# Kernel optimization log

Measured on AMD Instinct MI355X. Metric: run time of the kernel, lower is better.

Reference implementation:

```python
import jax, jax.numpy as jnp
import numpy as np

B, T, D = 4, 2048, 1024
H = 16
HD = D // H  # 64

def setup_inputs() -> dict:
    key = jax.random.key(0)
    ks = jax.random.split(key, 7)
    s = 1.0 / np.sqrt(D)
    x = jax.random.normal(ks[0], (B, T, D), dtype=jnp.float32)
    # Per-head query projections stacked: Wq[h] maps D -> HD
    Wq = jax.random.uniform(ks[1], (H, D, HD), minval=-s, maxval=s, dtype=jnp.float32)
    bq = jax.random.uniform(ks[2], (H, HD), minval=-s, maxval=s, dtype=jnp.float32)
    Wk = jax.random.uniform(ks[3], (D, HD), minval=-s, maxval=s, dtype=jnp.float32)
    bk = jax.random.uniform(ks[4], (HD,), minval=-s, maxval=s, dtype=jnp.float32)
    Wv = jax.random.uniform(ks[5], (D, HD), minval=-s, maxval=s, dtype=jnp.float32)
    bv = jax.random.uniform(ks[6], (HD,), minval=-s, maxval=s, dtype=jnp.float32)
    return {"x": x, "Wq": Wq, "bq": bq, "Wk": Wk, "bk": bk, "Wv": Wv, "bv": bv}

def reference(x, Wq, bq, Wk, bk, Wv, bv):
    # shared single K/V head: [B, T, HD]
    k = jnp.einsum('btd,de->bte', x, Wk) + bk
    v = jnp.einsum('btd,de->bte', x, Wv) + bv
    # per-head queries batched: [B, H, T, HD]
    q = jnp.einsum('btd,hde->bhte', x, Wq) + bq[:, None, :]
    scale = 1.0 / jnp.sqrt(jnp.asarray(HD, dtype=x.dtype))
    scores = jnp.einsum('bhqe,bke->bhqk', q, k) * scale  # [B, H, T, T]
    attn = jax.nn.softmax(scores, axis=-1)
    out = jnp.einsum('bhqk,bke->bhqe', attn, v)  # [B, H, T, HD]
    # concat heads along last dim (head order matches torch cat order)
    return jnp.transpose(out, (0, 2, 1, 3)).reshape(B, T, H * HD)
```

## Files before the change

kernel.cpp:

```cpp
#include <hip/hip_runtime.h>

#define B 4
#define T 2048
#define D 1024
#define H 16
#define HD 64
#define NKT 32

typedef __attribute__((ext_vector_type(8))) short bf16x8;
typedef __attribute__((ext_vector_type(4))) float f32x4;
typedef __attribute__((ext_vector_type(16))) float f32x16;

#define MFMA16(a, b, c) __builtin_amdgcn_mfma_f32_16x16x32_bf16(a, b, c, 0, 0, 0)
#define MFMA32(a, b, c) __builtin_amdgcn_mfma_f32_32x32x16_bf16(a, b, c, 0, 0, 0)

static __device__ __forceinline__ unsigned short f2bf(float f) {
    union { float f; unsigned u; } v; v.f = f;
    unsigned r = v.u + 0x7FFFu + ((v.u >> 16) & 1u);
    return (unsigned short)(r >> 16);
}

static __device__ __forceinline__ bf16x8 cvt8(const float* p) {
    float4 a = *(const float4*)p;
    float4 b = *(const float4*)(p + 4);
    bf16x8 r;
    r[0] = (short)f2bf(a.x); r[1] = (short)f2bf(a.y);
    r[2] = (short)f2bf(a.z); r[3] = (short)f2bf(a.w);
    r[4] = (short)f2bf(b.x); r[5] = (short)f2bf(b.y);
    r[6] = (short)f2bf(b.z); r[7] = (short)f2bf(b.w);
    return r;
}

static __device__ __forceinline__ unsigned cvtpk(float lo, float hi) {
    unsigned r;
    asm("v_cvt_pk_bf16_f32 %0, %1, %2" : "=v"(r) : "v"(lo), "v"(hi));
    return r;
}

static __device__ __forceinline__ f32x16 zero16() {
    f32x16 z;
#pragma unroll
    for (int i = 0; i < 16; ++i) z[i] = 0.f;
    return z;
}

static __device__ __forceinline__ float xhalf_sum(float x) {
    unsigned u = __float_as_uint(x);
    auto r = __builtin_amdgcn_permlane32_swap(u, u, false, false);
    return __uint_as_float(r[0]) + __uint_as_float(r[1]);
}

typedef __attribute__((address_space(1))) const unsigned char gl_u8;
typedef __attribute__((address_space(3))) unsigned char lds_u8;

static __device__ __forceinline__ void stage16(const void* g, void* l) {
    __builtin_amdgcn_global_load_lds((gl_u8*)(unsigned long long)g,
                                     (lds_u8*)(unsigned int)(unsigned long long)l,
                                     16, 0, 0);
}

__global__ __launch_bounds__(256) void pack_w(const float* __restrict__ Wq,
                                              const float* __restrict__ Wk,
                                              const float* __restrict__ Wv,
                                              unsigned short* __restrict__ Wqt,
                                              unsigned short* __restrict__ Wkt,
                                              unsigned short* __restrict__ Wvt) {
    __shared__ float tile[64][65];
    int hh = blockIdx.x >> 4, db = blockIdx.x & 15;
    const float* src;
    unsigned short* dst;
    if (hh < 16)      { src = Wq + (size_t)hh * D * HD; dst = Wqt + (size_t)hh * HD * D; }
    else if (hh == 16){ src = Wk; dst = Wkt; }
    else              { src = Wv; dst = Wvt; }
    int r = threadIdx.x >> 6, c = threadIdx.x & 63;
    int d0 = db * 64;
#pragma unroll
    for (int i = 0; i < 16; ++i)
        tile[r * 16 + i][c] = src[(size_t)(d0 + r * 16 + i) * HD + c];
    __syncthreads();
#pragma unroll
    for (int j = 0; j < 16; ++j)
        dst[(size_t)(r * 16 + j) * D + d0 + c] = f2bf(tile[c][r * 16 + j]);
}

__global__ __launch_bounds__(256) void kv_gemm(const float* __restrict__ xf,
                                               const unsigned short* __restrict__ Wkt,
                                               const unsigned short* __restrict__ Wvt,
                                               const float* __restrict__ bk,
                                               const float* __restrict__ bv,
                                               unsigned short* __restrict__ xbf,
                                               unsigned char* __restrict__ Ksw,
                                               unsigned char* __restrict__ Vsw) {
    int rt  = blockIdx.x * 2 + (threadIdx.x >> 7);
    int grp = (threadIdx.x >> 6) & 1;
    int lane = threadIdx.x & 63;
    int ln = lane & 15, lk = lane >> 4;
    int t0 = rt * 16;

    const unsigned short* Wt = grp ? Wvt : Wkt;
    const float* bias = grp ? bv : bk;

    f32x4 acc[4];
#pragma unroll
    for (int e = 0; e < 4; ++e) acc[e] = (f32x4){0.f, 0.f, 0.f, 0.f};

    for (int d0 = 0; d0 < D; d0 += 32) {
        size_t xi = (size_t)(t0 + ln) * D + d0 + lk * 8;
        bf16x8 a = cvt8(xf + xi);
        if (grp == 0) *(bf16x8*)(xbf + xi) = a;
#pragma unroll
        for (int e = 0; e < 4; ++e) {
            bf16x8 w = *(const bf16x8*)(Wt + (size_t)(e * 16 + ln) * D + d0 + lk * 8);
            acc[e] = MFMA16(a, w, acc[e]);
        }
    }

#pragma unroll
    for (int e = 0; e < 4; ++e)
#pragma unroll
        for (int r = 0; r < 4; ++r) {
            int trow = t0 + lk * 4 + r;
            float val = acc[e][r] + bias[e * 16 + ln];
            int bb = trow >> 11, tl = trow & 2047;
            size_t tbase = ((size_t)(bb * NKT + (tl >> 6))) << 13;
            int key = tl & 63;
            if (grp == 0) {
                int off = (e * 2 + (key >> 5)) * 1024 +
                          ((ln >> 3) * 32 + (key & 31)) * 16 + (ln & 7) * 2;
                *(unsigned short*)(Ksw + tbase + off) = f2bf(val);
            } else {
                int off = ((key >> 4) * 2 + (e >> 1)) * 1024 +
                          (((key >> 3) & 1) * 32 + (e & 1) * 16 + ln) * 16 +
                          (key & 7) * 2;
                *(unsigned short*)(Vsw + tbase + off) = f2bf(val);
            }
        }
}

__global__ __launch_bounds__(256, 4) void attn(const unsigned short* __restrict__ xbf,
                                               const unsigned short* __restrict__ Wqt,
                                               const float* __restrict__ bq,
                                               const unsigned char* __restrict__ Ksw,
                                               const unsigned char* __restrict__ Vsw,
                                               float* __restrict__ out) {
    __shared__ __align__(16) unsigned char smem[32768];

    int blk = ((blockIdx.x & 7) << 7) | (blockIdx.x >> 3);
    int qt = blk & 15;
    int h  = (blk >> 4) & 15;
    int b  = blk >> 8;
    int wave = threadIdx.x >> 6, lane = threadIdx.x & 63;
    int l31 = lane & 31, hi = lane >> 5;
    int t0 = qt * 128 + wave * 32;

    const unsigned char* Kt = Ksw + (((size_t)b * NKT) << 13);
    const unsigned char* Vt = Vsw + (((size_t)b * NKT) << 13);
    int soff = wave * 1024 + lane * 16;
    int ldsw = wave * 1024;

    auto STAGE = [&](int kt, int lk, int lv) {
        const unsigned char* gK = Kt + ((size_t)kt << 13);
        const unsigned char* gV = Vt + ((size_t)kt << 13);
        stage16(gK + soff,        smem + lk + ldsw);
        stage16(gK + 4096 + soff, smem + lk + 4096 + ldsw);
        stage16(gV + soff,        smem + lv + ldsw);
        stage16(gV + 4096 + soff, smem + lv + 4096 + ldsw);
    };

    STAGE(0, 0, 16384);

    f32x16 qacc[2] = {zero16(), zero16()};
    const unsigned short* Wh = Wqt + (size_t)h * HD * D;
    const unsigned short* xrow  = xbf + (size_t)(b * T + t0 + l31) * D + hi * 8;
    const unsigned short* wrow0 = Wh + (size_t)l31 * D + hi * 8;
    const unsigned short* wrow1 = Wh + (size_t)(32 + l31) * D + hi * 8;
    for (int dk = 0; dk < D; dk += 16) {
        bf16x8 xb = *(const bf16x8*)(xrow + dk);
        qacc[0] = MFMA32(*(const bf16x8*)(wrow0 + dk), xb, qacc[0]);
        qacc[1] = MFMA32(*(const bf16x8*)(wrow1 + dk), xb, qacc[1]);
    }

    const float sl2 = 0.125f * 1.44269504f;
    float qv[2][16];
#pragma unroll
    for (int e0 = 0; e0 < 2; ++e0)
#pragma unroll
        for (int r = 0; r < 16; ++r) {
            int crow = (r & 3) + 8 * (r >> 2) + 4 * hi;
            qv[e0][r] = (qacc[e0][r] + bq[h * HD + e0 * 32 + crow]) * sl2;
        }

    bf16x8 qf[4];
#pragma unroll
    for (int dt = 0; dt < 4; ++dt) {
        int s = dt >> 1;
        int b0 = 8 * (dt & 1), b1 = b0 + 4;
        unsigned c0 = cvtpk(qv[s][b0 + 0], qv[s][b0 + 1]);
        unsigned c1 = cvtpk(qv[s][b0 + 2], qv[s][b0 + 3]);
        unsigned c2 = cvtpk(qv[s][b1 + 0], qv[s][b1 + 1]);
        unsigned c3 = cvtpk(qv[s][b1 + 2], qv[s][b1 + 3]);
        auto r02 = __builtin_amdgcn_permlane32_swap(c0, c2, false, false);
        auto r13 = __builtin_amdgcn_permlane32_swap(c1, c3, false, false);
        union { unsigned u[4]; bf16x8 v; } pu;
        pu.u[0] = r02[0]; pu.u[1] = r13[0]; pu.u[2] = r02[1]; pu.u[3] = r13[1];
        qf[dt] = pu.v;
    }

    const unsigned char* fbase = smem + lane * 16;

    __syncthreads();

    f32x4 lr4 = (f32x4){0.f, 0.f, 0.f, 0.f};
    f32x16 o[2] = {zero16(), zero16()};

    auto PHASE = [&](int ck, int cv, int ph) {
        f32x16 s = zero16();
#pragma unroll
        for (int dt = 0; dt < 4; ++dt) {
            bf16x8 kf = *(const bf16x8*)(fbase + ck + (dt * 2 + ph) * 1024);
            s = MFMA32(kf, qf[dt], s);
        }

#pragma unroll
        for (int r = 0; r < 16; ++r)
            s[r] = __builtin_amdgcn_exp2f(s[r]);

#pragma unroll
        for (int i = 0; i < 4; ++i)
            lr4[i] += (s[i] + s[i + 8]) + (s[i + 4] + s[i + 12]);

#pragma unroll
        for (int ks = 0; ks < 2; ++ks) {
            int b0 = 8 * ks, b1 = b0 + 4;
            bf16x8 vf0 = *(const bf16x8*)(fbase + cv + ((ph * 2 + ks) * 2 + 0) * 1024);
            bf16x8 vf1 = *(const bf16x8*)(fbase + cv + ((ph * 2 + ks) * 2 + 1) * 1024);
            unsigned c0 = cvtpk(s[b0 + 0], s[b0 + 1]);
            unsigned c1 = cvtpk(s[b0 + 2], s[b0 + 3]);
            unsigned c2 = cvtpk(s[b1 + 0], s[b1 + 1]);
            unsigned c3 = cvtpk(s[b1 + 2], s[b1 + 3]);
            auto r02 = __builtin_amdgcn_permlane32_swap(c0, c2, false, false);
            auto r13 = __builtin_amdgcn_permlane32_swap(c1, c3, false, false);
            union { unsigned u[4]; bf16x8 v; } pu;
            pu.u[0] = r02[0]; pu.u[1] = r13[0]; pu.u[2] = r02[1]; pu.u[3] = r13[1];
            o[0] = MFMA32(vf0, pu.v, o[0]);
            o[1] = MFMA32(vf1, pu.v, o[1]);
        }
    };

    auto TILE = [&](int ck, int cv, int nxt, int nk, int nv) {
        if (nxt < NKT) STAGE(nxt, nk, nv);
        PHASE(ck, cv, 0);
        PHASE(ck, cv, 1);
        __syncthreads();
    };

    for (int kt = 0; kt < NKT; kt += 2) {
        TILE(0,    16384, kt + 1, 8192, 24576);
        TILE(8192, 24576, kt + 2, 0,    16384);
    }

    float lrun = xhalf_sum((lr4[0] + lr4[1]) + (lr4[2] + lr4[3]));
    float inv = 1.f / lrun;
    unsigned char* eb = smem + wave * 8192;
#pragma unroll
    for (int e0 = 0; e0 < 2; ++e0)
#pragma unroll
        for (int r = 0; r < 16; ++r) {
            int crow = (r & 3) + 8 * (r >> 2) + 4 * hi;
            int col4 = (e0 * 32 + crow) * 4;
            *(float*)(eb + l31 * 256 + (col4 ^ ((l31 & 15) << 4))) = o[e0][r] * inv;
        }
    __syncthreads();

    int rgrp = lane >> 4;
    int c16 = (lane & 15) * 16;
#pragma unroll
    for (int g = 0; g < 8; ++g) {
        int row = g * 4 + rgrp;
        float4 vv = *(const float4*)(eb + row * 256 + (c16 ^ ((row & 15) << 4)));
        *(float4*)(out + (size_t)(b * T + t0 + row) * D + h * HD + (c16 >> 2)) = vv;
    }
}

extern "C" void kernel_launch(void* const* d_in, const int* in_sizes, int n_in,
                              void* d_out, int out_size, void* d_ws, size_t ws_size,
                              hipStream_t stream) {
    const float* x  = (const float*)d_in[0];
    const float* Wq = (const float*)d_in[1];
    const float* bq = (const float*)d_in[2];
    const float* Wk = (const float*)d_in[3];
    const float* bk = (const float*)d_in[4];
    const float* Wv = (const float*)d_in[5];
    const float* bv = (const float*)d_in[6];
    float* out = (float*)d_out;

    unsigned char* ws = (unsigned char*)d_ws;
    unsigned short* xbf = (unsigned short*)(ws);
    unsigned short* Wqt = (unsigned short*)(ws + 16777216);
    unsigned short* Wkt = (unsigned short*)(ws + 18874368);
    unsigned short* Wvt = (unsigned short*)(ws + 19005440);
    unsigned char*  Ksw = ws + 19136512;
    unsigned char*  Vsw = ws + 20185088;

    pack_w<<<288, 256, 0, stream>>>(Wq, Wk, Wv, Wqt, Wkt, Wvt);
    kv_gemm<<<256, 256, 0, stream>>>(x, Wkt, Wvt, bk, bv, xbf, Ksw, Vsw);
    attn<<<1024, 256, 0, stream>>>(xbf, Wqt, bq, Ksw, Vsw, out);
}
```

Before: 172.6 us.

## Process two heads per 512-thread block sharing K/V tiles; store output directly

Each block now runs 8 waves covering two heads for the same 128 query rows. The K/V tiles staged in shared memory are reused by both heads, so each wave stages half as much data and total K/V global traffic per block pair is halved. The epilogue drops the LDS transpose and barrier and writes float4 output straight from the MFMA accumulators, which gives less coalesced 16-byte stores. Launch bounds move to 512 threads with no minimum-occupancy hint, which may change register allocation and occupancy.

Measured after the change: 170.9 us (median of 3 runs). No clear change (-1.0%).

```diff
diff --git a/kernel.cpp b/kernel.cpp
--- a/kernel.cpp
+++ b/kernel.cpp
@@ -137,34 +137,30 @@
         }
 }
 
-__global__ __launch_bounds__(256, 4) void attn(const unsigned short* __restrict__ xbf,
-                                               const unsigned short* __restrict__ Wqt,
-                                               const float* __restrict__ bq,
-                                               const unsigned char* __restrict__ Ksw,
-                                               const unsigned char* __restrict__ Vsw,
-                                               float* __restrict__ out) {
+__global__ __launch_bounds__(512) void attn(const unsigned short* __restrict__ xbf,
+                                            const unsigned short* __restrict__ Wqt,
+                                            const float* __restrict__ bq,
+                                            const unsigned char* __restrict__ Ksw,
+                                            const unsigned char* __restrict__ Vsw,
+                                            float* __restrict__ out) {
     __shared__ __align__(16) unsigned char smem[32768];
 
-    int blk = ((blockIdx.x & 7) << 7) | (blockIdx.x >> 3);
+    int blk = ((blockIdx.x & 7) << 6) | (blockIdx.x >> 3);
     int qt = blk & 15;
-    int h  = (blk >> 4) & 15;
-    int b  = blk >> 8;
+    int hp = (blk >> 4) & 7;
+    int b  = blk >> 7;
     int wave = threadIdx.x >> 6, lane = threadIdx.x & 63;
     int l31 = lane & 31, hi = lane >> 5;
-    int t0 = qt * 128 + wave * 32;
+    int h  = hp * 2 + (wave >> 2);
+    int t0 = qt * 128 + (wave & 3) * 32;
 
     const unsigned char* Kt = Ksw + (((size_t)b * NKT) << 13);
     const unsigned char* Vt = Vsw + (((size_t)b * NKT) << 13);
     int soff = wave * 1024 + lane * 16;
-    int ldsw = wave * 1024;
 
     auto STAGE = [&](int kt, int lk, int lv) {
-        const unsigned char* gK = Kt + ((size_t)kt << 13);
-        const unsigned char* gV = Vt + ((size_t)kt << 13);
-        stage16(gK + soff,        smem + lk + ldsw);
-        stage16(gK + 4096 + soff, smem + lk + 4096 + ldsw);
-        stage16(gV + soff,        smem + lv + ldsw);
-        stage16(gV + 4096 + soff, smem + lv + 4096 + ldsw);
+        stage16(Kt + ((size_t)kt << 13) + soff, smem + lk + soff);
+        stage16(Vt + ((size_t)kt << 13) + soff, smem + lv + soff);
     };
 
     STAGE(0, 0, 16384);
@@ -261,25 +257,18 @@
 
     float lrun = xhalf_sum((lr4[0] + lr4[1]) + (lr4[2] + lr4[3]));
     float inv = 1.f / lrun;
-    unsigned char* eb = smem + wave * 8192;
+    float* orow = out + (size_t)(b * T + t0 + l31) * D + h * HD + 4 * hi;
 #pragma unroll
     for (int e0 = 0; e0 < 2; ++e0)
 #pragma unroll
-        for (int r = 0; r < 16; ++r) {
-            int crow = (r & 3) + 8 * (r >> 2) + 4 * hi;
-            int col4 = (e0 * 32 + crow) * 4;
-            *(float*)(eb + l31 * 256 + (col4 ^ ((l31 & 15) << 4))) = o[e0][r] * inv;
-        }
-    __syncthreads();
-
-    int rgrp = lane >> 4;
-    int c16 = (lane & 15) * 16;
-#pragma unroll
-    for (int g = 0; g < 8; ++g) {
-        int row = g * 4 + rgrp;
-        float4 vv = *(const float4*)(eb + row * 256 + (c16 ^ ((row & 15) << 4)));
-        *(float4*)(out + (size_t)(b * T + t0 + row) * D + h * HD + (c16 >> 2)) = vv;
-    }
+        for (int g = 0; g < 4; ++g) {
+            float4 vv;
+            vv.x = o[e0][g * 4 + 0] * inv;
+            vv.y = o[e0][g * 4 + 1] * inv;
+            vv.z = o[e0][g * 4 + 2] * inv;
+            vv.w = o[e0][g * 4 + 3] * inv;
+            *(float4*)(orow + e0 * 32 + g * 8) = vv;
+        }
 }
 
 extern "C" void kernel_launch(void* const* d_in, const int* in_sizes, int n_in,
@@ -304,5 +293,5 @@
 
     pack_w<<<288, 256, 0, stream>>>(Wq, Wk, Wv, Wqt, Wkt, Wvt);
     kv_gemm<<<256, 256, 0, stream>>>(x, Wkt, Wvt, bk, bv, xbf, Ksw, Vsw);
-    attn<<<1024, 256, 0, stream>>>(xbf, Wqt, bq, Ksw, Vsw, out);
-}
+    attn<<<512, 512, 0, stream>>>(xbf, Wqt, bq, Ksw, Vsw, out);
+}
```
